# Performance work log

Hardware: AMD Instinct MI355X
Metric: run time of the kernel (lower is better)

Reference implementation:

```python
import jax, jax.numpy as jnp
import numpy as np

SEQ_LEN = 128
EMBED_DIM = 1024
BATCH = 128


def setup_inputs() -> dict:
    key = jax.random.key(0)
    ks = jax.random.split(key, 9)
    d = EMBED_DIM
    s = 0.02
    return {
        "x": jax.random.normal(ks[0], (BATCH, SEQ_LEN * d), dtype=jnp.float32),
        "Wq": jax.random.normal(ks[1], (d, d), dtype=jnp.float32) * s,
        "bq": jax.random.normal(ks[2], (d,), dtype=jnp.float32) * s,
        "Wk": jax.random.normal(ks[3], (d, d), dtype=jnp.float32) * s,
        "bk": jax.random.normal(ks[4], (d,), dtype=jnp.float32) * s,
        "Wv": jax.random.normal(ks[5], (d, d), dtype=jnp.float32) * s,
        "bv": jax.random.normal(ks[6], (d,), dtype=jnp.float32) * s,
        "Wo": jax.random.normal(ks[7], (d, d), dtype=jnp.float32) * s,
        "bo": jax.random.normal(ks[8], (d,), dtype=jnp.float32) * s,
    }


def reference(x, Wq, bq, Wk, bk, Wv, bv, Wo, bo):
    b = x.shape[0]
    d = EMBED_DIM
    xs = x.reshape(b, SEQ_LEN, d)  # [B, S, D]
    # torch Linear: y = x @ W.T + b
    Q = jnp.einsum("bsd,ed->bse", xs, Wq) + bq
    K = jnp.einsum("bsd,ed->bse", xs, Wk) + bk
    V = jnp.einsum("bsd,ed->bse", xs, Wv) + bv
    scores = jnp.einsum("bse,bte->bst", Q, K) / jnp.sqrt(jnp.float32(d))
    weights = jax.nn.softmax(scores, axis=-1)
    attended = jnp.einsum("bst,bte->bse", weights, V)
    out = jnp.einsum("bse,fe->bsf", attended, Wo) + bo
    return out.reshape(b, -1)
```

## Files before the change

### kernel.cpp

```cpp
#include <hip/hip_runtime.h>
#include <hip/hip_bf16.h>

typedef __attribute__((ext_vector_type(8))) __bf16 bf16x8;
typedef __attribute__((ext_vector_type(4))) __bf16 bf16x4;
typedef __attribute__((ext_vector_type(4))) float f32x4;

#define SEQ 128
#define DIM 1024
#define BATCH 128
#define MTOT (BATCH * SEQ)

__device__ __forceinline__ void gload16(const void* g, void* l) {
    __builtin_amdgcn_global_load_lds(
        (const __attribute__((address_space(1))) void*)g,
        (__attribute__((address_space(3))) void*)l, 16, 0, 0);
}

#define BARRIER() do { asm volatile("" ::: "memory"); __builtin_amdgcn_s_barrier(); asm volatile("" ::: "memory"); } while (0)
#define WAITV(N) asm volatile("s_waitcnt vmcnt(" #N ")" ::: "memory")
#define MFMA(a, b, c) __builtin_amdgcn_mfma_f32_16x16x32_bf16(a, b, c, 0, 0, 0)

__global__ void cast_w4(const float* __restrict__ a, const float* __restrict__ b,
                        const float* __restrict__ c, const float* __restrict__ d,
                        __bf16* __restrict__ oa, __bf16* __restrict__ ob,
                        __bf16* __restrict__ oc, __bf16* __restrict__ od, int n) {
    const float* src; __bf16* dst;
    switch (blockIdx.y) {
        case 0: src = a; dst = oa; break;
        case 1: src = b; dst = ob; break;
        case 2: src = c; dst = oc; break;
        default: src = d; dst = od; break;
    }
    int i = (blockIdx.x * blockDim.x + threadIdx.x) * 8;
    if (i >= n) return;
    float4 f0 = *reinterpret_cast<const float4*>(src + i);
    float4 f1 = *reinterpret_cast<const float4*>(src + i + 4);
    bf16x8 o;
    o[0] = (__bf16)f0.x; o[1] = (__bf16)f0.y; o[2] = (__bf16)f0.z; o[3] = (__bf16)f0.w;
    o[4] = (__bf16)f1.x; o[5] = (__bf16)f1.y; o[6] = (__bf16)f1.z; o[7] = (__bf16)f1.w;
    *reinterpret_cast<bf16x8*>(dst + i) = o;
}

__device__ __forceinline__ bf16x8 ldfa(const char* bufA, int R, int ks32) {
    const int sw = (R & 7) << 4;
    f32x4 lo = *reinterpret_cast<const f32x4*>(bufA + ((R * 128 + ks32) ^ sw));
    f32x4 hi = *reinterpret_cast<const f32x4*>(bufA + ((R * 128 + ks32 + 16) ^ sw));
    bf16x8 o;
    o[0] = (__bf16)lo[0]; o[1] = (__bf16)lo[1]; o[2] = (__bf16)lo[2]; o[3] = (__bf16)lo[3];
    o[4] = (__bf16)hi[0]; o[5] = (__bf16)hi[1]; o[6] = (__bf16)hi[2]; o[7] = (__bf16)hi[3];
    return o;
}

__global__ __launch_bounds__(512, 1) void gemm_qkv(const float* __restrict__ X,
        const __bf16* __restrict__ Wqb, const __bf16* __restrict__ Wkb, const __bf16* __restrict__ Wvb,
        const float* __restrict__ bq, const float* __restrict__ bk, const float* __restrict__ bv,
        __bf16* __restrict__ Qo, __bf16* __restrict__ Ko, __bf16* __restrict__ Vt) {
    __shared__ char lds[3][49152];
    const int tid = threadIdx.x, wave = tid >> 6, lane = tid & 63;
    const int wr = wave >> 2, wc = wave & 3;
    const int lr = lane & 15;
    const int lkb  = ((lane >> 4) & 3) * 16;
    const int ks32 = ((lane >> 4) & 3) * 32;
    const unsigned bid = blockIdx.x;
    const unsigned swz = (bid & 7) * 96 + (bid >> 3);
    const int mt = swz / 12, nt = swz % 12;
    const int m0 = mt * 256;
    const int n0row = (nt & 3) * 256;
    const int mid = nt >> 2;
    const __bf16* Wsel = (mid == 0) ? Wqb : (mid == 1) ? Wkb : Wvb;
    const float*  bsel = (mid == 0) ? bq  : (mid == 1) ? bk  : bv;

    const int csrcA = ((lane & 7) * 16) ^ (((lane >> 3) & 7) << 4);
    const int cbsB  = ((lane & 3) * 16) ^ (((lane >> 3) & 3) << 4);
    const char* pAg = (const char*)X + (size_t)(m0 + wave * 32 + (lane >> 3)) * 4096 + csrcA;
    const char* pBg = (const char*)Wsel + (size_t)(n0row + wave * 32 + (lane >> 2)) * 2048 + cbsB;

    f32x4 acc[8][4] = {};

#define QLDFB(R) (*reinterpret_cast<const bf16x8*>(bufB + (R) * 64 + (lkb ^ ((((R) >> 1) & 3) << 4))))
#define QSTAGE_A(SB, TS) do { char* d_ = &lds[SB][0] + wave * 4096; const char* s_ = pAg + (size_t)(TS) * 128; \
    gload16(s_, d_); gload16(s_ + 8 * 4096, d_ + 1024); \
    gload16(s_ + 16 * 4096, d_ + 2048); gload16(s_ + 24 * 4096, d_ + 3072); } while (0)
#define QSTAGE_B(SB, TS) do { char* d_ = &lds[SB][32768] + wave * 2048; const char* s_ = pBg + (size_t)(TS) * 64; \
    gload16(s_, d_); gload16(s_ + 16 * 2048, d_ + 1024); } while (0)

#define QTILE(RB, SB, TS, DOSTAGE, VMSTMT) do { \
    const char* bufA = &lds[RB][0]; \
    const char* bufB = &lds[RB][32768]; \
    bf16x8 a0 = ldfa(bufA, wr * 128 + 0 * 16 + lr, ks32), a1 = ldfa(bufA, wr * 128 + 1 * 16 + lr, ks32); \
    bf16x8 a2 = ldfa(bufA, wr * 128 + 2 * 16 + lr, ks32), a3 = ldfa(bufA, wr * 128 + 3 * 16 + lr, ks32); \
    bf16x8 b0 = QLDFB(wc * 64 + 0 * 16 + lr), b1 = QLDFB(wc * 64 + 1 * 16 + lr); \
    bf16x8 b2 = QLDFB(wc * 64 + 2 * 16 + lr), b3 = QLDFB(wc * 64 + 3 * 16 + lr); \
    if (DOSTAGE) QSTAGE_A(SB, TS); \
    BARRIER(); \
    __builtin_amdgcn_s_setprio(1); \
    acc[0][0] = MFMA(a0, b0, acc[0][0]); acc[0][1] = MFMA(a0, b1, acc[0][1]); \
    acc[0][2] = MFMA(a0, b2, acc[0][2]); acc[0][3] = MFMA(a0, b3, acc[0][3]); \
    acc[1][0] = MFMA(a1, b0, acc[1][0]); acc[1][1] = MFMA(a1, b1, acc[1][1]); \
    acc[1][2] = MFMA(a1, b2, acc[1][2]); acc[1][3] = MFMA(a1, b3, acc[1][3]); \
    acc[2][0] = MFMA(a2, b0, acc[2][0]); acc[2][1] = MFMA(a2, b1, acc[2][1]); \
    acc[2][2] = MFMA(a2, b2, acc[2][2]); acc[2][3] = MFMA(a2, b3, acc[2][3]); \
    acc[3][0] = MFMA(a3, b0, acc[3][0]); acc[3][1] = MFMA(a3, b1, acc[3][1]); \
    acc[3][2] = MFMA(a3, b2, acc[3][2]); acc[3][3] = MFMA(a3, b3, acc[3][3]); \
    __builtin_amdgcn_s_setprio(0); \
    BARRIER(); \
    a0 = ldfa(bufA, wr * 128 + 64 + 0 * 16 + lr, ks32); a1 = ldfa(bufA, wr * 128 + 64 + 1 * 16 + lr, ks32); \
    a2 = ldfa(bufA, wr * 128 + 64 + 2 * 16 + lr, ks32); a3 = ldfa(bufA, wr * 128 + 64 + 3 * 16 + lr, ks32); \
    if (DOSTAGE) QSTAGE_B(SB, TS); \
    BARRIER(); \
    __builtin_amdgcn_s_setprio(1); \
    acc[4][0] = MFMA(a0, b0, acc[4][0]); acc[4][1] = MFMA(a0, b1, acc[4][1]); \
    acc[4][2] = MFMA(a0, b2, acc[4][2]); acc[4][3] = MFMA(a0, b3, acc[4][3]); \
    acc[5][0] = MFMA(a1, b0, acc[5][0]); acc[5][1] = MFMA(a1, b1, acc[5][1]); \
    acc[5][2] = MFMA(a1, b2, acc[5][2]); acc[5][3] = MFMA(a1, b3, acc[5][3]); \
    acc[6][0] = MFMA(a2, b0, acc[6][0]); acc[6][1] = MFMA(a2, b1, acc[6][1]); \
    acc[6][2] = MFMA(a2, b2, acc[6][2]); acc[6][3] = MFMA(a2, b3, acc[6][3]); \
    acc[7][0] = MFMA(a3, b0, acc[7][0]); acc[7][1] = MFMA(a3, b1, acc[7][1]); \
    acc[7][2] = MFMA(a3, b2, acc[7][2]); acc[7][3] = MFMA(a3, b3, acc[7][3]); \
    __builtin_amdgcn_s_setprio(0); \
    VMSTMT; \
    BARRIER(); \
} while (0)

    QSTAGE_A(0, 0); QSTAGE_B(0, 0);
    QSTAGE_A(1, 1); QSTAGE_B(1, 1);
    WAITV(6);
    BARRIER();

    for (int it = 0; it < 10; ++it) {
        const int t = it * 3;
        QTILE(0, 2, t + 2, 1, WAITV(6));
        QTILE(1, 0, t + 3, 1, WAITV(6));
        QTILE(2, 1, t + 4, 1, WAITV(6));
    }
    QTILE(0, 0, 0, 0, WAITV(0));
    QTILE(1, 0, 0, 0, (void)0);

    const int rbase = (lane >> 4) * 4;
    #pragma unroll
    for (int ri = 0; ri < 8; ++ri) {
        #pragma unroll
        for (int j = 0; j < 4; ++j) {
            const int gcl = n0row + wc * 64 + j * 16 + lr;
            const float bvv = bsel[gcl];
            const int grb = m0 + wr * 128 + ri * 16 + rbase;
            if (mid < 2) {
                __bf16* C = (mid == 0) ? Qo : Ko;
                #pragma unroll
                for (int r = 0; r < 4; ++r)
                    C[(size_t)(grb + r) * DIM + gcl] = (__bf16)(acc[ri][j][r] + bvv);
            } else {
                const int b = grb >> 7, s = grb & 127;
                bf16x4 v;
                #pragma unroll
                for (int r = 0; r < 4; ++r) v[r] = (__bf16)(acc[ri][j][r] + bvv);
                *reinterpret_cast<bf16x4*>(&Vt[((size_t)b * DIM + gcl) * SEQ + s]) = v;
            }
        }
    }
#undef QTILE
#undef QSTAGE_A
#undef QSTAGE_B
#undef QLDFB
}

template <int MODE>
__global__ __launch_bounds__(512, 1) void gemm256(const __bf16* __restrict__ A,
                                                  const __bf16* __restrict__ W,
                                                  const float* __restrict__ bias,
                                                  void* __restrict__ Cout) {
    const int K = 1024, N = 1024;
    __shared__ __bf16 lds[3][4][4096];
    const int tid = threadIdx.x, wave = tid >> 6, lane = tid & 63;
    const int wr = wave >> 2, wc = wave & 3;
    const int lr = lane & 15;
    const int lkb = ((lane >> 4) & 3) * 16;
    const int bid = blockIdx.x;
    const int swz = (bid & 7) * 32 + (bid >> 3);
    const int m0 = (swz >> 2) * 256, n0 = (swz & 3) * 256;
    const int rloc = wave * 16 + (lane >> 2);
    const int cbs  = ((((lane & 3) << 4) ^ (((lane >> 3) & 3) << 4)) >> 1);
    const __bf16* pA = A + (size_t)(m0 + rloc) * K + cbs;
    const __bf16* pB = W + (size_t)(n0 + rloc) * K + cbs;
    const int wo = wave * 512;

    f32x4 acc[8][4] = {};

#define LDF(SLOT, R) (*reinterpret_cast<const bf16x8*>( \
        reinterpret_cast<const char*>(SLOT) + (R) * 64 + (lkb ^ ((((R) >> 1) & 3) << 4))))
#define STAGE_A(SB, TS) do { gload16(pA + (TS) * 32, &lds[SB][0][wo]); \
                             gload16(pA + (size_t)128 * 1024 + (TS) * 32, &lds[SB][1][wo]); } while (0)
#define STAGE_B(SB, TS) do { gload16(pB + (TS) * 32, &lds[SB][2][wo]); \
                             gload16(pB + (size_t)128 * 1024 + (TS) * 32, &lds[SB][3][wo]); } while (0)

#define TILE(RB, SB, TS, DOSTAGE, VMSTMT) do { \
    const __bf16* As_ = &lds[RB][wr][0]; \
    const __bf16* Bs_ = &lds[RB][2 + (wc >> 1)][0]; \
    const int bb_ = (wc & 1) * 64; \
    bf16x8 a0 = LDF(As_, 0 * 16 + lr), a1 = LDF(As_, 1 * 16 + lr); \
    bf16x8 a2 = LDF(As_, 2 * 16 + lr), a3 = LDF(As_, 3 * 16 + lr); \
    bf16x8 b0 = LDF(Bs_, bb_ + 0 * 16 + lr), b1 = LDF(Bs_, bb_ + 1 * 16 + lr); \
    bf16x8 b2 = LDF(Bs_, bb_ + 2 * 16 + lr), b3 = LDF(Bs_, bb_ + 3 * 16 + lr); \
    if (DOSTAGE) STAGE_A(SB, TS); \
    BARRIER(); \
    __builtin_amdgcn_s_setprio(1); \
    acc[0][0] = MFMA(a0, b0, acc[0][0]); acc[0][1] = MFMA(a0, b1, acc[0][1]); \
    acc[0][2] = MFMA(a0, b2, acc[0][2]); acc[0][3] = MFMA(a0, b3, acc[0][3]); \
    acc[1][0] = MFMA(a1, b0, acc[1][0]); acc[1][1] = MFMA(a1, b1, acc[1][1]); \
    acc[1][2] = MFMA(a1, b2, acc[1][2]); acc[1][3] = MFMA(a1, b3, acc[1][3]); \
    acc[2][0] = MFMA(a2, b0, acc[2][0]); acc[2][1] = MFMA(a2, b1, acc[2][1]); \
    acc[2][2] = MFMA(a2, b2, acc[2][2]); acc[2][3] = MFMA(a2, b3, acc[2][3]); \
    acc[3][0] = MFMA(a3, b0, acc[3][0]); acc[3][1] = MFMA(a3, b1, acc[3][1]); \
    acc[3][2] = MFMA(a3, b2, acc[3][2]); acc[3][3] = MFMA(a3, b3, acc[3][3]); \
    __builtin_amdgcn_s_setprio(0); \
    BARRIER(); \
    a0 = LDF(As_, 4 * 16 + lr); a1 = LDF(As_, 5 * 16 + lr); \
    a2 = LDF(As_, 6 * 16 + lr); a3 = LDF(As_, 7 * 16 + lr); \
    if (DOSTAGE) STAGE_B(SB, TS); \
    BARRIER(); \
    __builtin_amdgcn_s_setprio(1); \
    acc[4][0] = MFMA(a0, b0, acc[4][0]); acc[4][1] = MFMA(a0, b1, acc[4][1]); \
    acc[4][2] = MFMA(a0, b2, acc[4][2]); acc[4][3] = MFMA(a0, b3, acc[4][3]); \
    acc[5][0] = MFMA(a1, b0, acc[5][0]); acc[5][1] = MFMA(a1, b1, acc[5][1]); \
    acc[5][2] = MFMA(a1, b2, acc[5][2]); acc[5][3] = MFMA(a1, b3, acc[5][3]); \
    acc[6][0] = MFMA(a2, b0, acc[6][0]); acc[6][1] = MFMA(a2, b1, acc[6][1]); \
    acc[6][2] = MFMA(a2, b2, acc[6][2]); acc[6][3] = MFMA(a2, b3, acc[6][3]); \
    acc[7][0] = MFMA(a3, b0, acc[7][0]); acc[7][1] = MFMA(a3, b1, acc[7][1]); \
    acc[7][2] = MFMA(a3, b2, acc[7][2]); acc[7][3] = MFMA(a3, b3, acc[7][3]); \
    __builtin_amdgcn_s_setprio(0); \
    VMSTMT; \
    BARRIER(); \
} while (0)

    STAGE_A(0, 0); STAGE_B(0, 0);
    STAGE_A(1, 1); STAGE_B(1, 1);
    WAITV(4);
    BARRIER();

    for (int it = 0; it < 10; ++it) {
        const int t = it * 3;
        TILE(0, 2, t + 2, 1, WAITV(4));
        TILE(1, 0, t + 3, 1, WAITV(4));
        TILE(2, 1, t + 4, 1, WAITV(4));
    }
    TILE(0, 0, 0, 0, WAITV(0));
    TILE(1, 0, 0, 0, (void)0);

    const int rbase = (lane >> 4) * 4;
    #pragma unroll
    for (int ri = 0; ri < 8; ++ri) {
        #pragma unroll
        for (int j = 0; j < 4; ++j) {
            const int gc  = n0 + wc * 64 + j * 16 + lr;
            const float bv = bias[gc];
            const int grb = m0 + wr * 128 + ri * 16 + rbase;
            if (MODE == 0) {
                __bf16* C = (__bf16*)Cout;
                #pragma unroll
                for (int r = 0; r < 4; ++r)
                    C[(size_t)(grb + r) * N + gc] = (__bf16)(acc[ri][j][r] + bv);
            } else if (MODE == 1) {
                float* C = (float*)Cout;
                #pragma unroll
                for (int r = 0; r < 4; ++r)
                    C[(size_t)(grb + r) * N + gc] = acc[ri][j][r] + bv;
            } else {
                __bf16* C = (__bf16*)Cout;
                const int b = grb >> 7, s = grb & 127;
                bf16x4 v;
                #pragma unroll
                for (int r = 0; r < 4; ++r) v[r] = (__bf16)(acc[ri][j][r] + bv);
                *reinterpret_cast<bf16x4*>(&C[((size_t)b * DIM + gc) * SEQ + s]) = v;
            }
        }
    }
#undef TILE
#undef STAGE_A
#undef STAGE_B
#undef LDF
}

__global__ __launch_bounds__(256) void attn_kernel(const __bf16* __restrict__ Q,
                                                   const __bf16* __restrict__ Km,
                                                   const __bf16* __restrict__ Vt,
                                                   __bf16* __restrict__ Ab) {
    __shared__ __align__(16) char smem[40960];
    float  (*Ssh)[132] = (float(*)[132])(smem);
    __bf16 (*Psh)[136] = (__bf16(*)[136])(smem + 16896);

    const int bid = blockIdx.x;
    const int logical = (bid & 7) * 64 + (bid >> 3);
    const int b = logical >> 2, rt = logical & 3;
    const int tid = threadIdx.x, wave = tid >> 6, lane = tid & 63;
    const int lr = lane & 15, lk = (lane >> 4) * 8, rbase = (lane >> 4) * 4;
    const __bf16* Qb = Q  + ((size_t)b * SEQ + rt * 32) * DIM;
    const __bf16* Kb = Km + (size_t)b * SEQ * DIM;
    const __bf16* Vb = Vt + (size_t)b * DIM * SEQ;

    const int csrc = ((lane & 7) * 16) ^ (((lane >> 3) & 7) << 4);

    f32x4 acc[2][2] = {};
    {
        auto stage_kq = [&](int buf, int c) {
            char* Kd = smem + buf * 20480 + wave * 4096;
            char* Qd = smem + buf * 20480 + 16384 + wave * 1024;
            const char* Ks = (const char*)Kb + (size_t)(wave * 32 + (lane >> 3)) * 2048 + c * 128 + csrc;
            #pragma unroll
            for (int q = 0; q < 4; ++q)
                gload16(Ks + (size_t)q * 8 * 2048, Kd + q * 1024);
            const char* Qs = (const char*)Qb + (size_t)(wave * 8 + (lane >> 3)) * 2048 + c * 128 + csrc;
            gload16(Qs, Qd);
        };
        stage_kq(0, 0);
        WAITV(0);
        BARRIER();
        for (int c = 0; c < 16; ++c) {
            const int rb = c & 1;
            if (c < 15) stage_kq(rb ^ 1, c + 1);
            const char* Kl = smem + rb * 20480;
            const char* Ql = Kl + 16384;
            bf16x8 qf[2][2], kf[2][2];
            #pragma unroll
            for (int i = 0; i < 2; ++i)
                #pragma unroll
                for (int ks = 0; ks < 2; ++ks) {
                    const int r = i * 16 + lr;
                    qf[i][ks] = *reinterpret_cast<const bf16x8*>(
                        Ql + r * 128 + ((ks * 64 + (lane >> 4) * 16) ^ ((r & 7) << 4)));
                }
            #pragma unroll
            for (int j = 0; j < 2; ++j)
                #pragma unroll
                for (int ks = 0; ks < 2; ++ks) {
                    const int r = wave * 32 + j * 16 + lr;
                    kf[j][ks] = *reinterpret_cast<const bf16x8*>(
                        Kl + r * 128 + ((ks * 64 + (lane >> 4) * 16) ^ ((r & 7) << 4)));
                }
            __builtin_amdgcn_s_setprio(1);
            #pragma unroll
            for (int i = 0; i < 2; ++i)
                #pragma unroll
                for (int j = 0; j < 2; ++j)
                    #pragma unroll
                    for (int ks = 0; ks < 2; ++ks)
                        acc[i][j] = MFMA(qf[i][ks], kf[j][ks], acc[i][j]);
            __builtin_amdgcn_s_setprio(0);
            WAITV(0);
            BARRIER();
        }
    }
    const float scale = 0.03125f;
    #pragma unroll
    for (int i = 0; i < 2; ++i)
        #pragma unroll
        for (int j = 0; j < 2; ++j)
            #pragma unroll
            for (int r = 0; r < 4; ++r)
                Ssh[i * 16 + rbase + r][wave * 32 + j * 16 + lr] = acc[i][j][r] * scale;
    __syncthreads();

    {
        const int row = tid >> 3;
        const int c0  = (tid & 7) * 16;
        float4 v0 = *reinterpret_cast<const float4*>(&Ssh[row][c0]);
        float4 v1 = *reinterpret_cast<const float4*>(&Ssh[row][c0 + 4]);
        float4 v2 = *reinterpret_cast<const float4*>(&Ssh[row][c0 + 8]);
        float4 v3 = *reinterpret_cast<const float4*>(&Ssh[row][c0 + 12]);
        float e[16] = {v0.x, v0.y, v0.z, v0.w, v1.x, v1.y, v1.z, v1.w,
                       v2.x, v2.y, v2.z, v2.w, v3.x, v3.y, v3.z, v3.w};
        float mx = e[0];
        #pragma unroll
        for (int u = 1; u < 16; ++u) mx = fmaxf(mx, e[u]);
        mx = fmaxf(mx, __shfl_xor(mx, 1));
        mx = fmaxf(mx, __shfl_xor(mx, 2));
        mx = fmaxf(mx, __shfl_xor(mx, 4));
        float s = 0.f;
        #pragma unroll
        for (int u = 0; u < 16; ++u) { e[u] = __expf(e[u] - mx); s += e[u]; }
        s += __shfl_xor(s, 1);
        s += __shfl_xor(s, 2);
        s += __shfl_xor(s, 4);
        const float inv = 1.f / s;
        bf16x8 p0, p1;
        #pragma unroll
        for (int u = 0; u < 8; ++u) { p0[u] = (__bf16)(e[u] * inv); p1[u] = (__bf16)(e[u + 8] * inv); }
        *reinterpret_cast<bf16x8*>(&Psh[row][c0])     = p0;
        *reinterpret_cast<bf16x8*>(&Psh[row][c0 + 8]) = p1;
    }
    __syncthreads();

    bf16x8 pf[2][4];
    #pragma unroll
    for (int i = 0; i < 2; ++i)
        #pragma unroll
        for (int ks = 0; ks < 4; ++ks)
            pf[i][ks] = *reinterpret_cast<const bf16x8*>(&Psh[i * 16 + lr][ks * 32 + lk]);
    __syncthreads();

    __bf16* Ao = Ab + ((size_t)b * SEQ + rt * 32) * DIM;
    {
        auto stage_v = [&](int buf, int c) {
            char* Vd = smem + buf * 16384 + wave * 4096;
            #pragma unroll
            for (int q = 0; q < 4; ++q) {
                const int rowl = wave * 16 + q * 4 + (lane >> 4);
                const char* Vs = (const char*)Vb + (size_t)(c * 64 + rowl) * 256 +
                                 (((lane & 15) * 16) ^ ((rowl & 7) << 4));
                gload16(Vs, Vd + q * 1024);
            }
        };
        stage_v(0, 0);
        WAITV(0);
        BARRIER();
        for (int c = 0; c < 16; ++c) {
            const int rb = c & 1;
            if (c < 15) stage_v(rb ^ 1, c + 1);
            const char* Vl = smem + rb * 16384;
            f32x4 a2[2] = {};
            const int r = wave * 16 + lr;
            #pragma unroll
            for (int ks = 0; ks < 4; ++ks) {
                bf16x8 vf = *reinterpret_cast<const bf16x8*>(
                    Vl + r * 256 + ((ks * 64 + (lane >> 4) * 16) ^ ((r & 7) << 4)));
                a2[0] = MFMA(pf[0][ks], vf, a2[0]);
                a2[1] = MFMA(pf[1][ks], vf, a2[1]);
            }
            const int n0 = c * 64 + wave * 16;
            #pragma unroll
            for (int i = 0; i < 2; ++i)
                #pragma unroll
                for (int rr = 0; rr < 4; ++rr)
                    Ao[(size_t)(i * 16 + rbase + rr) * DIM + n0 + lr] = (__bf16)a2[i][rr];
            WAITV(8);
            BARRIER();
        }
    }
}

extern "C" void kernel_launch(void* const* d_in, const int* in_sizes, int n_in,
                              void* d_out, int out_size, void* d_ws, size_t ws_size,
                              hipStream_t stream) {
    const float* x  = (const float*)d_in[0];
    const float* Wq = (const float*)d_in[1];
    const float* bq = (const float*)d_in[2];
    const float* Wk = (const float*)d_in[3];
    const float* bk = (const float*)d_in[4];
    const float* Wv = (const float*)d_in[5];
    const float* bv = (const float*)d_in[6];
    const float* Wo = (const float*)d_in[7];
    const float* bo = (const float*)d_in[8];

    char* ws = (char*)d_ws;
    const size_t MB = 1024 * 1024;
    __bf16* Ab  = (__bf16*)(ws);
    __bf16* Wqb = (__bf16*)(ws + 32 * MB);
    __bf16* Wkb = (__bf16*)(ws + 34 * MB);
    __bf16* Wvb = (__bf16*)(ws + 36 * MB);
    __bf16* Wob = (__bf16*)(ws + 38 * MB);
    __bf16* Qb  = (__bf16*)(ws + 40 * MB);
    __bf16* Kb  = (__bf16*)(ws + 72 * MB);
    __bf16* Vt  = (__bf16*)(ws + 104 * MB);

    const int nW = DIM * DIM;
    cast_w4<<<dim3(nW / 8 / 256, 4), 256, 0, stream>>>(Wq, Wk, Wv, Wo, Wqb, Wkb, Wvb, Wob, nW);

    gemm_qkv<<<768, 512, 0, stream>>>(x, Wqb, Wkb, Wvb, bq, bk, bv, Qb, Kb, Vt);

    attn_kernel<<<512, 256, 0, stream>>>(Qb, Kb, Vt, Ab);

    gemm256<1><<<256, 512, 0, stream>>>(Ab, Wob, bo, d_out);
}
```

Baseline: 220.6 us.

## Pre-cast X to bf16 in a separate pass before QKV GEMM

Adds a cast pass that converts the fp32 input X to bf16 in the workspace alongside the weight casts. The QKV GEMM now streams bf16 A tiles using the same staging layout as gemm256, replacing in-loop fp32-to-bf16 conversion and halving A-tile LDS and global traffic per k-step. In exchange it adds an extra full write and read of a 32MB bf16 copy of X. The workspace buffer previously used for attention output is reused to hold X in bf16.

```diff
diff --git a/kernel.cpp b/kernel.cpp
--- a/kernel.cpp
+++ b/kernel.cpp
@@ -20,19 +20,24 @@
 #define WAITV(N) asm volatile("s_waitcnt vmcnt(" #N ")" ::: "memory")
 #define MFMA(a, b, c) __builtin_amdgcn_mfma_f32_16x16x32_bf16(a, b, c, 0, 0, 0)
 
-__global__ void cast_w4(const float* __restrict__ a, const float* __restrict__ b,
-                        const float* __restrict__ c, const float* __restrict__ d,
-                        __bf16* __restrict__ oa, __bf16* __restrict__ ob,
-                        __bf16* __restrict__ oc, __bf16* __restrict__ od, int n) {
-    const float* src; __bf16* dst;
-    switch (blockIdx.y) {
-        case 0: src = a; dst = oa; break;
-        case 1: src = b; dst = ob; break;
-        case 2: src = c; dst = oc; break;
-        default: src = d; dst = od; break;
-    }
-    int i = (blockIdx.x * blockDim.x + threadIdx.x) * 8;
-    if (i >= n) return;
+__global__ void cast_all(const float* __restrict__ x,
+                         const float* __restrict__ Wq, const float* __restrict__ Wk,
+                         const float* __restrict__ Wv, const float* __restrict__ Wo,
+                         __bf16* __restrict__ Xb,
+                         __bf16* __restrict__ Wqb, __bf16* __restrict__ Wkb,
+                         __bf16* __restrict__ Wvb, __bf16* __restrict__ Wob) {
+    const float* src; __bf16* dst; size_t base;
+    if (blockIdx.y == 0) {
+        src = x; dst = Xb; base = (size_t)blockIdx.x * 2048;
+    } else {
+        const int j = blockIdx.x;
+        if (j >= 2048) return;
+        const int w = j >> 9;
+        src = (w == 0) ? Wq : (w == 1) ? Wk : (w == 2) ? Wv : Wo;
+        dst = (w == 0) ? Wqb : (w == 1) ? Wkb : (w == 2) ? Wvb : Wob;
+        base = (size_t)(j & 511) * 2048;
+    }
+    const size_t i = base + (size_t)threadIdx.x * 8;
     float4 f0 = *reinterpret_cast<const float4*>(src + i);
     float4 f1 = *reinterpret_cast<const float4*>(src + i + 4);
     bf16x8 o;
@@ -41,26 +46,16 @@
     *reinterpret_cast<bf16x8*>(dst + i) = o;
 }
 
-__device__ __forceinline__ bf16x8 ldfa(const char* bufA, int R, int ks32) {
-    const int sw = (R & 7) << 4;
-    f32x4 lo = *reinterpret_cast<const f32x4*>(bufA + ((R * 128 + ks32) ^ sw));
-    f32x4 hi = *reinterpret_cast<const f32x4*>(bufA + ((R * 128 + ks32 + 16) ^ sw));
-    bf16x8 o;
-    o[0] = (__bf16)lo[0]; o[1] = (__bf16)lo[1]; o[2] = (__bf16)lo[2]; o[3] = (__bf16)lo[3];
-    o[4] = (__bf16)hi[0]; o[5] = (__bf16)hi[1]; o[6] = (__bf16)hi[2]; o[7] = (__bf16)hi[3];
-    return o;
-}
-
-__global__ __launch_bounds__(512, 1) void gemm_qkv(const float* __restrict__ X,
+__global__ __launch_bounds__(512, 1) void gemm_qkv3(const __bf16* __restrict__ A,
         const __bf16* __restrict__ Wqb, const __bf16* __restrict__ Wkb, const __bf16* __restrict__ Wvb,
         const float* __restrict__ bq, const float* __restrict__ bk, const float* __restrict__ bv,
         __bf16* __restrict__ Qo, __bf16* __restrict__ Ko, __bf16* __restrict__ Vt) {
-    __shared__ char lds[3][49152];
+    const int K = 1024;
+    __shared__ __bf16 lds[3][4][4096];
     const int tid = threadIdx.x, wave = tid >> 6, lane = tid & 63;
     const int wr = wave >> 2, wc = wave & 3;
     const int lr = lane & 15;
-    const int lkb  = ((lane >> 4) & 3) * 16;
-    const int ks32 = ((lane >> 4) & 3) * 32;
+    const int lkb = ((lane >> 4) & 3) * 16;
     const unsigned bid = blockIdx.x;
     const unsigned swz = (bid & 7) * 96 + (bid >> 3);
     const int mt = swz / 12, nt = swz % 12;
@@ -70,28 +65,30 @@
     const __bf16* Wsel = (mid == 0) ? Wqb : (mid == 1) ? Wkb : Wvb;
     const float*  bsel = (mid == 0) ? bq  : (mid == 1) ? bk  : bv;
 
-    const int csrcA = ((lane & 7) * 16) ^ (((lane >> 3) & 7) << 4);
-    const int cbsB  = ((lane & 3) * 16) ^ (((lane >> 3) & 3) << 4);
-    const char* pAg = (const char*)X + (size_t)(m0 + wave * 32 + (lane >> 3)) * 4096 + csrcA;
-    const char* pBg = (const char*)Wsel + (size_t)(n0row + wave * 32 + (lane >> 2)) * 2048 + cbsB;
+    const int rloc = wave * 16 + (lane >> 2);
+    const int cbs  = ((((lane & 3) << 4) ^ (((lane >> 3) & 3) << 4)) >> 1);
+    const __bf16* pA = A + (size_t)(m0 + rloc) * K + cbs;
+    const __bf16* pB = Wsel + (size_t)(n0row + rloc) * K + cbs;
+    const int wo = wave * 512;
 
     f32x4 acc[8][4] = {};
 
-#define QLDFB(R) (*reinterpret_cast<const bf16x8*>(bufB + (R) * 64 + (lkb ^ ((((R) >> 1) & 3) << 4))))
-#define QSTAGE_A(SB, TS) do { char* d_ = &lds[SB][0] + wave * 4096; const char* s_ = pAg + (size_t)(TS) * 128; \
-    gload16(s_, d_); gload16(s_ + 8 * 4096, d_ + 1024); \
-    gload16(s_ + 16 * 4096, d_ + 2048); gload16(s_ + 24 * 4096, d_ + 3072); } while (0)
-#define QSTAGE_B(SB, TS) do { char* d_ = &lds[SB][32768] + wave * 2048; const char* s_ = pBg + (size_t)(TS) * 64; \
-    gload16(s_, d_); gload16(s_ + 16 * 2048, d_ + 1024); } while (0)
-
-#define QTILE(RB, SB, TS, DOSTAGE, VMSTMT) do { \
-    const char* bufA = &lds[RB][0]; \
-    const char* bufB = &lds[RB][32768]; \
-    bf16x8 a0 = ldfa(bufA, wr * 128 + 0 * 16 + lr, ks32), a1 = ldfa(bufA, wr * 128 + 1 * 16 + lr, ks32); \
-    bf16x8 a2 = ldfa(bufA, wr * 128 + 2 * 16 + lr, ks32), a3 = ldfa(bufA, wr * 128 + 3 * 16 + lr, ks32); \
-    bf16x8 b0 = QLDFB(wc * 64 + 0 * 16 + lr), b1 = QLDFB(wc * 64 + 1 * 16 + lr); \
-    bf16x8 b2 = QLDFB(wc * 64 + 2 * 16 + lr), b3 = QLDFB(wc * 64 + 3 * 16 + lr); \
-    if (DOSTAGE) QSTAGE_A(SB, TS); \
+#define LDF(SLOT, R) (*reinterpret_cast<const bf16x8*>( \
+        reinterpret_cast<const char*>(SLOT) + (R) * 64 + (lkb ^ ((((R) >> 1) & 3) << 4))))
+#define STAGE_A(SB, TS) do { gload16(pA + (TS) * 32, &lds[SB][0][wo]); \
+                             gload16(pA + (size_t)128 * 1024 + (TS) * 32, &lds[SB][1][wo]); } while (0)
+#define STAGE_B(SB, TS) do { gload16(pB + (TS) * 32, &lds[SB][2][wo]); \
+                             gload16(pB + (size_t)128 * 1024 + (TS) * 32, &lds[SB][3][wo]); } while (0)
+
+#define TILE(RB, SB, TS, DOSTAGE, VMSTMT) do { \
+    const __bf16* As_ = &lds[RB][wr][0]; \
+    const __bf16* Bs_ = &lds[RB][2 + (wc >> 1)][0]; \
+    const int bb_ = (wc & 1) * 64; \
+    bf16x8 a0 = LDF(As_, 0 * 16 + lr), a1 = LDF(As_, 1 * 16 + lr); \
+    bf16x8 a2 = LDF(As_, 2 * 16 + lr), a3 = LDF(As_, 3 * 16 + lr); \
+    bf16x8 b0 = LDF(Bs_, bb_ + 0 * 16 + lr), b1 = LDF(Bs_, bb_ + 1 * 16 + lr); \
+    bf16x8 b2 = LDF(Bs_, bb_ + 2 * 16 + lr), b3 = LDF(Bs_, bb_ + 3 * 16 + lr); \
+    if (DOSTAGE) STAGE_A(SB, TS); \
     BARRIER(); \
     __builtin_amdgcn_s_setprio(1); \
     acc[0][0] = MFMA(a0, b0, acc[0][0]); acc[0][1] = MFMA(a0, b1, acc[0][1]); \
@@ -104,9 +101,9 @@
     acc[3][2] = MFMA(a3, b2, acc[3][2]); acc[3][3] = MFMA(a3, b3, acc[3][3]); \
     __builtin_amdgcn_s_setprio(0); \
     BARRIER(); \
-    a0 = ldfa(bufA, wr * 128 + 64 + 0 * 16 + lr, ks32); a1 = ldfa(bufA, wr * 128 + 64 + 1 * 16 + lr, ks32); \
-    a2 = ldfa(bufA, wr * 128 + 64 + 2 * 16 + lr, ks32); a3 = ldfa(bufA, wr * 128 + 64 + 3 * 16 + lr, ks32); \
-    if (DOSTAGE) QSTAGE_B(SB, TS); \
+    a0 = LDF(As_, 4 * 16 + lr); a1 = LDF(As_, 5 * 16 + lr); \
+    a2 = LDF(As_, 6 * 16 + lr); a3 = LDF(As_, 7 * 16 + lr); \
+    if (DOSTAGE) STAGE_B(SB, TS); \
     BARRIER(); \
     __builtin_amdgcn_s_setprio(1); \
     acc[4][0] = MFMA(a0, b0, acc[4][0]); acc[4][1] = MFMA(a0, b1, acc[4][1]); \
@@ -122,19 +119,19 @@
     BARRIER(); \
 } while (0)
 
-    QSTAGE_A(0, 0); QSTAGE_B(0, 0);
-    QSTAGE_A(1, 1); QSTAGE_B(1, 1);
-    WAITV(6);
+    STAGE_A(0, 0); STAGE_B(0, 0);
+    STAGE_A(1, 1); STAGE_B(1, 1);
+    WAITV(4);
     BARRIER();
 
     for (int it = 0; it < 10; ++it) {
         const int t = it * 3;
-        QTILE(0, 2, t + 2, 1, WAITV(6));
-        QTILE(1, 0, t + 3, 1, WAITV(6));
-        QTILE(2, 1, t + 4, 1, WAITV(6));
-    }
-    QTILE(0, 0, 0, 0, WAITV(0));
-    QTILE(1, 0, 0, 0, (void)0);
+        TILE(0, 2, t + 2, 1, WAITV(4));
+        TILE(1, 0, t + 3, 1, WAITV(4));
+        TILE(2, 1, t + 4, 1, WAITV(4));
+    }
+    TILE(0, 0, 0, 0, WAITV(0));
+    TILE(1, 0, 0, 0, (void)0);
 
     const int rbase = (lane >> 4) * 4;
     #pragma unroll
@@ -158,10 +155,10 @@
             }
         }
     }
-#undef QTILE
-#undef QSTAGE_A
-#undef QSTAGE_B
-#undef QLDFB
+#undef TILE
+#undef STAGE_A
+#undef STAGE_B
+#undef LDF
 }
 
 template <int MODE>
@@ -452,7 +449,7 @@
 
     char* ws = (char*)d_ws;
     const size_t MB = 1024 * 1024;
-    __bf16* Ab  = (__bf16*)(ws);
+    __bf16* Xb  = (__bf16*)(ws);
     __bf16* Wqb = (__bf16*)(ws + 32 * MB);
     __bf16* Wkb = (__bf16*)(ws + 34 * MB);
     __bf16* Wvb = (__bf16*)(ws + 36 * MB);
@@ -460,11 +457,11 @@
     __bf16* Qb  = (__bf16*)(ws + 40 * MB);
     __bf16* Kb  = (__bf16*)(ws + 72 * MB);
     __bf16* Vt  = (__bf16*)(ws + 104 * MB);
-
-    const int nW = DIM * DIM;
-    cast_w4<<<dim3(nW / 8 / 256, 4), 256, 0, stream>>>(Wq, Wk, Wv, Wo, Wqb, Wkb, Wvb, Wob, nW);
-
-    gemm_qkv<<<768, 512, 0, stream>>>(x, Wqb, Wkb, Wvb, bq, bk, bv, Qb, Kb, Vt);
+    __bf16* Ab  = Xb;
+
+    cast_all<<<dim3(8192, 2), 256, 0, stream>>>(x, Wq, Wk, Wv, Wo, Xb, Wqb, Wkb, Wvb, Wob);
+
+    gemm_qkv3<<<768, 512, 0, stream>>>(Xb, Wqb, Wkb, Wvb, bq, bk, bv, Qb, Kb, Vt);
 
     attn_kernel<<<512, 256, 0, stream>>>(Qb, Kb, Vt, Ab);
 
```

After: 189.7 us. -14.0%, faster.
